# Kernel optimization log

Measured on AMD Instinct MI355X. Metric: run time of the kernel, lower is better.

Reference implementation:

```python
import jax, jax.numpy as jnp
import numpy as np

H = 512      # hidden_size
NH = 8       # head_size (num heads)
DH = H // NH # att_size per head
FFN = 2048
B, S = 8, 1024
NEG = -1e9
EPS = 1e-5


def _layernorm(x, g, b):
    mu = jnp.mean(x, axis=-1, keepdims=True)
    var = jnp.var(x, axis=-1, keepdims=True)
    return (x - mu) * jax.lax.rsqrt(var + EPS) * g + b


def setup_inputs() -> dict:
    key = jax.random.key(0)
    ks = jax.random.split(key, 16)
    s = 0.02
    return {
        "x": jax.random.normal(ks[0], (B, S, H), jnp.float32),
        "attn_bias": jax.random.normal(ks[1], (B, S, S), jnp.float32),
        "graph_mask": jax.random.randint(ks[2], (B, S, S), 0, 2, jnp.int32),
        "ln1_g": jnp.ones((H,), jnp.float32),
        "ln1_b": jnp.zeros((H,), jnp.float32),
        "Wq": jax.random.normal(ks[3], (H, H), jnp.float32) * s,
        "bq": jnp.zeros((H,), jnp.float32),
        "Wk": jax.random.normal(ks[4], (H, H), jnp.float32) * s,
        "bk": jnp.zeros((H,), jnp.float32),
        "Wv": jax.random.normal(ks[5], (H, H), jnp.float32) * s,
        "bv": jnp.zeros((H,), jnp.float32),
        "Wo": jax.random.normal(ks[6], (H, H), jnp.float32) * s,
        "bo": jnp.zeros((H,), jnp.float32),
        "ln2_g": jnp.ones((H,), jnp.float32),
        "ln2_b": jnp.zeros((H,), jnp.float32),
        "W1": jax.random.normal(ks[7], (H, FFN), jnp.float32) * s,
        "b1": jnp.zeros((FFN,), jnp.float32),
        "W2": jax.random.normal(ks[8], (FFN, H), jnp.float32) * s,
        "b2": jnp.zeros((H,), jnp.float32),
    }


def reference(x, attn_bias, graph_mask, ln1_g, ln1_b, Wq, bq, Wk, bk, Wv, bv,
              Wo, bo, ln2_g, ln2_b, W1, b1, W2, b2):
    b, s, h = x.shape
    # --- self-attention block (eval mode: dropouts are identity) ---
    y = _layernorm(x, ln1_g, ln1_b)
    q = (y @ Wq + bq).reshape(b, s, NH, DH).transpose(0, 2, 1, 3)  # [B,h,S,d]
    k = (y @ Wk + bk).reshape(b, s, NH, DH).transpose(0, 2, 1, 3)
    v = (y @ Wv + bv).reshape(b, s, NH, DH).transpose(0, 2, 1, 3)
    scale = DH ** -0.5
    scores = jnp.einsum('bhqd,bhkd->bhqk', q * scale, k)  # [B,h,S,S]
    mask = (graph_mask == 0)[:, None, :, :]               # [B,1,S,S] broadcast over heads
    bias = jnp.where(mask, NEG, attn_bias[:, None, :, :])
    scores = scores + bias
    scores = jnp.where(mask, NEG, scores)
    p = jax.nn.softmax(scores, axis=-1)
    o = jnp.einsum('bhqk,bhkd->bhqd', p, v)
    o = o.transpose(0, 2, 1, 3).reshape(b, s, h) @ Wo + bo
    x = x + o
    # --- FFN block ---
    y = _layernorm(x, ln2_g, ln2_b)
    y = jax.nn.gelu(y @ W1 + b1, approximate=False) @ W2 + b2
    return x + y
```

## Files before the change

kernel.cpp:

```cpp
#include <hip/hip_runtime.h>
#include <hip/hip_bf16.h>
#include <type_traits>

static constexpr int kS   = 1024;
static constexpr int kH   = 512;
static constexpr int kFFN = 2048;

using bf16 = __hip_bfloat16;
using short8  = __attribute__((ext_vector_type(8))) short;
using float4v = __attribute__((ext_vector_type(4))) float;
#define MFMA16 __builtin_amdgcn_mfma_f32_16x16x32_bf16

__device__ __forceinline__ unsigned short f2bfu(float f){
  unsigned int u = __float_as_uint(f);
  return (unsigned short)((u + 0x7fffu + ((u >> 16) & 1u)) >> 16);
}
__device__ __forceinline__ float bfu2f(unsigned short u){
  return __uint_as_float(((unsigned int)u) << 16);
}
__device__ __forceinline__ unsigned int pack2(float a, float b){
  return (unsigned int)f2bfu(a) | ((unsigned int)f2bfu(b) << 16);
}
__device__ __forceinline__ void async16(const void* g, void* l){
  __builtin_amdgcn_global_load_lds(
    (const __attribute__((address_space(1))) unsigned int*)g,
    (__attribute__((address_space(3))) unsigned int*)l, 16, 0, 0);
}
__device__ __forceinline__ int swz(int col, int row){
  return (col & ~63) | (((((col>>3)&7) ^ (row&7)))<<3) | (col&7);
}

__global__ __launch_bounds__(256) void ln_kernel(const float* __restrict__ x,
    const float* __restrict__ g, const float* __restrict__ bb, bf16* __restrict__ y){
  int wave = threadIdx.x >> 6, lane = threadIdx.x & 63;
  long row = (long)blockIdx.x * 4 + wave;
  const float* xr = x + row * kH + lane*8;
  float4 a = *(const float4*)xr, c = *(const float4*)(xr+4);
  float v[8] = {a.x,a.y,a.z,a.w,c.x,c.y,c.z,c.w};
  float s=0.f, s2=0.f;
#pragma unroll
  for(int i=0;i<8;i++){ s += v[i]; s2 += v[i]*v[i]; }
#pragma unroll
  for(int o=32; o>=1; o>>=1){ s += __shfl_xor(s,o,64); s2 += __shfl_xor(s2,o,64); }
  float mu  = s * (1.f/kH);
  float rs  = rsqrtf(s2*(1.f/kH) - mu*mu + 1e-5f);
  float gv[8], bv[8];
  {
    float4 t0=*(const float4*)(g+lane*8),  t1=*(const float4*)(g+lane*8+4);
    float4 t2=*(const float4*)(bb+lane*8), t3=*(const float4*)(bb+lane*8+4);
    gv[0]=t0.x;gv[1]=t0.y;gv[2]=t0.z;gv[3]=t0.w;gv[4]=t1.x;gv[5]=t1.y;gv[6]=t1.z;gv[7]=t1.w;
    bv[0]=t2.x;bv[1]=t2.y;bv[2]=t2.z;bv[3]=t2.w;bv[4]=t3.x;bv[5]=t3.y;bv[6]=t3.z;bv[7]=t3.w;
  }
  unsigned int ow[4];
#pragma unroll
  for(int i=0;i<4;i++){
    float a0 = (v[2*i]  -mu)*rs*gv[2*i]   + bv[2*i];
    float a1 = (v[2*i+1]-mu)*rs*gv[2*i+1] + bv[2*i+1];
    ow[i] = pack2(a0, a1);
  }
  *reinterpret_cast<uint4*>(y + row*kH + swz(lane*8, (int)row)) = make_uint4(ow[0],ow[1],ow[2],ow[3]);
}

__global__ __launch_bounds__(256) void prep_wt(const float* __restrict__ W,
    bf16* __restrict__ WT, int K, int N){
  __shared__ unsigned short Ts[64*68];
  int tid=threadIdx.x;
  int kb=blockIdx.y*64, nb=blockIdx.x*64;
  {
    int k=tid>>2, nc=(tid&3)*16;
    const float* p = W + (size_t)(kb+k)*N + nb+nc;
#pragma unroll
    for(int i=0;i<16;i+=4){
      float4 f = *(const float4*)(p+i);
      Ts[k*68+nc+i  ]=f2bfu(f.x); Ts[k*68+nc+i+1]=f2bfu(f.y);
      Ts[k*68+nc+i+2]=f2bfu(f.z); Ts[k*68+nc+i+3]=f2bfu(f.w);
    }
  }
  __syncthreads();
  {
    int n=tid>>2, kc=(tid&3)*16;
    unsigned short tmp[16];
#pragma unroll
    for(int i=0;i<16;i++) tmp[i] = Ts[(kc+i)*68 + n];
    int row = nb+n, kg0 = kc>>3;
    bf16* op = WT + (size_t)row*K + kb;
    *(uint4*)(op + (((kg0  ^(row&7)))<<3)) = *(uint4*)&tmp[0];
    *(uint4*)(op + ((((kg0+1)^(row&7)))<<3)) = *(uint4*)&tmp[8];
  }
}

__global__ __launch_bounds__(256) void concat3(const float* __restrict__ a,
    const float* __restrict__ b, const float* __restrict__ c, float* __restrict__ o){
  int i = blockIdx.x*256 + threadIdx.x;
  if(i < 1536) o[i] = i<512 ? a[i] : (i<1024 ? b[i-512] : c[i-1024]);
}

__global__ __launch_bounds__(256) void bias_eff_kernel(
    const int* __restrict__ mask, const float* __restrict__ bias, bf16* __restrict__ be){
  size_t i8 = ((size_t)blockIdx.x*256 + threadIdx.x)*8;
  int4   m0 = *(const int4*)(mask+i8),   m1 = *(const int4*)(mask+i8+4);
  float4 b0 = *(const float4*)(bias+i8), b1 = *(const float4*)(bias+i8+4);
  const unsigned short NEG = f2bfu(-1e9f);
  unsigned short o[8];
  o[0]=m0.x?f2bfu(b0.x):NEG; o[1]=m0.y?f2bfu(b0.y):NEG;
  o[2]=m0.z?f2bfu(b0.z):NEG; o[3]=m0.w?f2bfu(b0.w):NEG;
  o[4]=m1.x?f2bfu(b1.x):NEG; o[5]=m1.y?f2bfu(b1.y):NEG;
  o[6]=m1.z?f2bfu(b1.z):NEG; o[7]=m1.w?f2bfu(b1.w):NEG;
  *(uint4*)((unsigned short*)be + i8) = *(uint4*)o;
}

__global__ __launch_bounds__(256) void transpose_bf16(
    const bf16* __restrict__ v, bf16* __restrict__ vT, int R)
{
  __shared__ unsigned short Ts[64*72];
  int tid=threadIdx.x;
  int rb = blockIdx.y*64, cb = blockIdx.x*64;
  {
    int r=tid>>2, c=(tid&3)*16;
    const bf16* p = v + (size_t)(rb+r)*kH + cb + c;
    *(uint4*)(&Ts[r*72+c])   = *(const uint4*)p;
    *(uint4*)(&Ts[r*72+c+8]) = *(const uint4*)(p+8);
  }
  __syncthreads();
  {
    int c=tid>>2, kb=(tid&3)*16;
    unsigned short tmp[16];
#pragma unroll
    for(int i=0;i<16;i++) tmp[i] = Ts[(kb+i)*72 + c];
    bf16* op = vT + (size_t)(cb+c)*R + rb + kb;
    *(uint4*)(op)   = *(uint4*)(&tmp[0]);
    *(uint4*)(op+8) = *(uint4*)(&tmp[8]);
  }
}

template<int BM, int BN, typename OutT, bool SCALE, bool GELU, bool RES, bool CSW>
__global__ __launch_bounds__((BM/64)*(BN/64)*64, 3) void mfma_gemm(
    const bf16* __restrict__ A, const bf16* __restrict__ BT,
    const float* __restrict__ bias, const float* __restrict__ res,
    OutT* __restrict__ C, int M, int N, int K)
{
  constexpr int W  = (BM/64)*(BN/64);
  constexpr int NW = BN/64;
  constexpr int AC = (BM/8)/W, BC = (BN/8)/W;
  __shared__ __align__(16) unsigned short As[BM*64];
  __shared__ __align__(16) unsigned short Bs[BN*64];
  int tid=threadIdx.x, lane=tid&63, quad=lane>>4, l16=lane&15;
  int w=__builtin_amdgcn_readfirstlane(tid>>6);
  int wr = w / NW, wc = w % NW;
  int m0=blockIdx.y*BM, n0=blockIdx.x*BN;
  int lr=lane>>3, lc=lane&7;
  float4v acc[4][4] = {};
  for(int k0=0;k0<K;k0+=64){
    __syncthreads();
#pragma unroll
    for(int i=0;i<AC;i++){
      int r = (w*AC+i)*8;
      async16(A + (size_t)(m0+r+lr)*K + k0 + lc*8, &As[r*64]);
    }
#pragma unroll
    for(int i=0;i<BC;i++){
      int r = (w*BC+i)*8;
      async16(BT + (size_t)(n0+r+lr)*K + k0 + lc*8, &Bs[r*64]);
    }
    __syncthreads();
#pragma unroll
    for(int hf=0;hf<2;hf++){
      short8 af[4], bfv[4];
#pragma unroll
      for(int mi=0;mi<4;mi++){
        int row=wr*64+mi*16+l16;
        af[mi]=*(const short8*)&As[row*64 + (((hf*4+quad)^(row&7))<<3)];
      }
#pragma unroll
      for(int ni=0;ni<4;ni++){
        int n=wc*64+ni*16+l16;
        bfv[ni]=*(const short8*)&Bs[n*64 + (((hf*4+quad)^(n&7))<<3)];
      }
#pragma unroll
      for(int ni=0;ni<4;ni++)
#pragma unroll
        for(int mi=0;mi<4;mi++)
          acc[mi][ni]=MFMA16(af[mi],bfv[ni],acc[mi][ni],0,0,0);
    }
  }
#pragma unroll
  for(int ni=0;ni<4;ni++){
    int col=n0+wc*64+ni*16+l16;
    float bc=bias[col];
#pragma unroll
    for(int mi=0;mi<4;mi++){
#pragma unroll
      for(int r=0;r<4;r++){
        int row=m0+wr*64+mi*16+quad*4+r;
        float v=acc[mi][ni][r]+bc;
        if constexpr(SCALE) v*=0.125f;
        if constexpr(GELU)  v=0.5f*v*(1.f+erff(v*0.70710678118f));
        size_t idx=(size_t)row*N+col;
        if constexpr(RES) v+=res[idx];
        if constexpr(std::is_same<OutT,float>::value) C[idx]=v;
        else {
          size_t ix = CSW ? ((size_t)row*N + swz(col,row)) : idx;
          reinterpret_cast<unsigned short*>(C)[ix]=f2bfu(v);
        }
      }
    }
  }
}

__global__ __launch_bounds__(256, 3) void mfma_gemm_qkv(
    const bf16* __restrict__ A, const bf16* __restrict__ BT,
    const float* __restrict__ bias, bf16* __restrict__ qo,
    bf16* __restrict__ ko, bf16* __restrict__ vo, int M, int N, int K)
{
  __shared__ __align__(16) unsigned short As[128*64];
  __shared__ __align__(16) unsigned short Bs[128*64];
  int tid=threadIdx.x, lane=tid&63, quad=lane>>4, l16=lane&15;
  int w=__builtin_amdgcn_readfirstlane(tid>>6);
  int wr = w >> 1, wc = w & 1;
  int m0=blockIdx.y*128, n0=blockIdx.x*128;
  int lr=lane>>3, lc=lane&7;
  float4v acc[4][4] = {};
  for(int k0=0;k0<K;k0+=64){
    __syncthreads();
#pragma unroll
    for(int i=0;i<4;i++){
      int r = (w*4+i)*8;
      async16(A + (size_t)(m0+r+lr)*K + k0 + lc*8, &As[r*64]);
    }
#pragma unroll
    for(int i=0;i<4;i++){
      int r = (w*4+i)*8;
      async16(BT + (size_t)(n0+r+lr)*K + k0 + lc*8, &Bs[r*64]);
    }
    __syncthreads();
#pragma unroll
    for(int hf=0;hf<2;hf++){
      short8 af[4], bfv[4];
#pragma unroll
      for(int mi=0;mi<4;mi++){
        int row=wr*64+mi*16+l16;
        af[mi]=*(const short8*)&As[row*64 + (((hf*4+quad)^(row&7))<<3)];
      }
#pragma unroll
      for(int ni=0;ni<4;ni++){
        int n=wc*64+ni*16+l16;
        bfv[ni]=*(const short8*)&Bs[n*64 + (((hf*4+quad)^(n&7))<<3)];
      }
#pragma unroll
      for(int ni=0;ni<4;ni++)
#pragma unroll
        for(int mi=0;mi<4;mi++)
          acc[mi][ni]=MFMA16(af[mi],bfv[ni],acc[mi][ni],0,0,0);
    }
  }
  int sec = __builtin_amdgcn_readfirstlane(n0 >> 9);
  unsigned short* dst = (unsigned short*)(sec==0 ? qo : (sec==1 ? ko : vo));
  float scl = (sec==0) ? 0.125f : 1.0f;
#pragma unroll
  for(int ni=0;ni<4;ni++){
    int col=n0+wc*64+ni*16+l16;
    float bc=bias[col];
    int cl=col&511;
#pragma unroll
    for(int mi=0;mi<4;mi++){
#pragma unroll
      for(int r=0;r<4;r++){
        int row=m0+wr*64+mi*16+quad*4+r;
        dst[(size_t)row*512+cl]=f2bfu((acc[mi][ni][r]+bc)*scl);
      }
    }
  }
}

__global__ __launch_bounds__(256,2) void attn_mfma(
    const bf16* __restrict__ q, const bf16* __restrict__ k,
    const bf16* __restrict__ vT, const bf16* __restrict__ be,
    bf16* __restrict__ o)
{
  __shared__ __align__(16) unsigned short Ks[64*64];
  __shared__ __align__(16) unsigned short Vt[64*64];
  __shared__ __align__(16) unsigned short Bt[64*64];
  __shared__ __align__(16) unsigned short Ps[4*16*72];
  int tid=threadIdx.x, lane=tid&63, quad=lane>>4, l16=lane&15;
  int w=__builtin_amdgcn_readfirstlane(tid>>6);
  int q0=blockIdx.x*64, b=blockIdx.y>>3, h=blockIdx.y&7;
  int lr=lane>>3, lc=lane&7;
  const bf16* qp = q + (size_t)(b*kS + q0 + w*16 + l16)*kH + h*64;
  short8 aq0 = *(const short8*)(qp + quad*8);
  short8 aq1 = *(const short8*)(qp + 32 + quad*8);
  float lpart[4]={0.f,0.f,0.f,0.f};
  float4v oacc[4]={};
  int pb = w*16*72;
  int rql = w*16 + quad*4;
  for(int kt=0;kt<16;kt++){
    int kb=kt*64;
    __syncthreads();
#pragma unroll
    for(int i=0;i<2;i++){
      int rr = w*16 + i*8;
      async16(k  + (size_t)(b*kS+kb+rr+lr)*kH + h*64 + ((lc^lr)<<3), &Ks[rr*64]);
      async16(vT + (size_t)(h*64+rr+lr)*8192 + b*kS + kb + ((lc^lr)<<3), &Vt[rr*64]);
      async16(be + (size_t)(b*kS+q0+rr+lr)*kS + kb + ((lc^lr)<<3), &Bt[rr*64]);
    }
    __syncthreads();
    float4v sa[4];
#pragma unroll
    for(int t=0;t<4;t++){
      int krow=t*16+l16, kx=krow&7;
      short8 b0 = *(const short8*)&Ks[krow*64 + ((quad^kx)<<3)];
      short8 b1 = *(const short8*)&Ks[krow*64 + (((4+quad)^kx)<<3)];
      float4v ci;
#pragma unroll
      for(int r=0;r<4;r++){
        int row = rql + r;
        ci[r] = bfu2f(Bt[row*64 + (((t*2+(l16>>3)) ^ (row&7))<<3) + (l16&7)]);
      }
      ci = MFMA16(aq0,b0,ci,0,0,0);
      sa[t]=MFMA16(aq1,b1,ci,0,0,0);
    }
#pragma unroll
    for(int t=0;t<4;t++){
      int kg = t*2 + (l16>>3), j = l16&7;
#pragma unroll
      for(int r=0;r<4;r++){
        float p = __expf(sa[t][r] - 24.f);
        lpart[r] += p;
        int row = quad*4+r;
        Ps[pb + row*72 + ((kg^(row&7))<<3) + j] = f2bfu(p);
      }
    }
    short8 ap0 = *(const short8*)&Ps[pb + l16*72 + ((quad^(l16&7))<<3)];
    short8 ap1 = *(const short8*)&Ps[pb + l16*72 + (((4+quad)^(l16&7))<<3)];
#pragma unroll
    for(int dt=0;dt<4;dt++){
      int vrow=dt*16+l16, vx=vrow&7;
      short8 bv0=*(const short8*)&Vt[vrow*64+((quad^vx)<<3)];
      short8 bv1=*(const short8*)&Vt[vrow*64+(((4+quad)^vx)<<3)];
      oacc[dt]=MFMA16(ap0,bv0,oacc[dt],0,0,0);
      oacc[dt]=MFMA16(ap1,bv1,oacc[dt],0,0,0);
    }
  }
  float inv[4];
#pragma unroll
  for(int r=0;r<4;r++){
    float l = lpart[r];
    l += __shfl_xor(l,1,64); l += __shfl_xor(l,2,64);
    l += __shfl_xor(l,4,64); l += __shfl_xor(l,8,64);
    inv[r] = 1.f/l;
  }
#pragma unroll
  for(int dt=0;dt<4;dt++)
#pragma unroll
    for(int r=0;r<4;r++){
      int row = b*kS + q0 + rql + r;
      int col = h*64 + dt*16 + l16;
      reinterpret_cast<unsigned short*>(o)[(size_t)row*kH + swz(col,row)] =
        f2bfu(oacc[dt][r]*inv[r]);
    }
}

extern "C" void kernel_launch(void* const* d_in, const int* in_sizes, int n_in,
                              void* d_out, int out_size, void* d_ws, size_t ws_size,
                              hipStream_t stream){
  (void)in_sizes; (void)n_in; (void)out_size; (void)ws_size;
  const float* x         = (const float*)d_in[0];
  const float* attn_bias = (const float*)d_in[1];
  const int*   graph_mask= (const int*)  d_in[2];
  const float* ln1_g = (const float*)d_in[3];
  const float* ln1_b = (const float*)d_in[4];
  const float* Wq = (const float*)d_in[5];
  const float* bq = (const float*)d_in[6];
  const float* Wk = (const float*)d_in[7];
  const float* bk = (const float*)d_in[8];
  const float* Wv = (const float*)d_in[9];
  const float* bv = (const float*)d_in[10];
  const float* Wo = (const float*)d_in[11];
  const float* bo = (const float*)d_in[12];
  const float* ln2_g = (const float*)d_in[13];
  const float* ln2_b = (const float*)d_in[14];
  const float* W1 = (const float*)d_in[15];
  const float* b1 = (const float*)d_in[16];
  const float* W2 = (const float*)d_in[17];
  const float* b2 = (const float*)d_in[18];

  char* wsb = (char*)d_ws;
  const size_t SZ = (size_t)8192 * kH * sizeof(bf16);
  bf16* s0 = (bf16*)(wsb);
  bf16* s1 = (bf16*)(wsb + SZ);
  bf16* s2 = (bf16*)(wsb + 2*SZ);
  bf16* s3 = (bf16*)(wsb + 3*SZ);
  float* outf = (float*)d_out;
  bf16*  WqkvT = (bf16*)d_out;
  float* bqkv  = (float*)((char*)d_out + (2u<<20));
  bf16*  vraw  = (bf16*)((char*)d_out + (8u<<20));
  bf16*  beP   = (bf16*)d_out;
  bf16* WoT = s3;
  bf16* W1T = s3 + 262144;
  bf16* W2T = s3 + 262144 + 1048576;

  dim3 blk(256);
  prep_wt<<<dim3(8,8),  blk, 0, stream>>>(Wq, WqkvT,          kH, kH);
  prep_wt<<<dim3(8,8),  blk, 0, stream>>>(Wk, WqkvT + 262144, kH, kH);
  prep_wt<<<dim3(8,8),  blk, 0, stream>>>(Wv, WqkvT + 524288, kH, kH);
  concat3<<<dim3(6), blk, 0, stream>>>(bq, bk, bv, bqkv);
  ln_kernel<<<dim3(2048), blk, 0, stream>>>(x, ln1_g, ln1_b, s0);
  mfma_gemm_qkv<<<dim3(12,64), blk, 0, stream>>>(s0, WqkvT, bqkv, s1, s2, vraw, 8192, 3*kH, kH);
  transpose_bf16<<<dim3(8,128), blk, 0, stream>>>(vraw, s3, 8192);
  bias_eff_kernel<<<dim3(4096), blk, 0, stream>>>(graph_mask, attn_bias, beP);
  attn_mfma<<<dim3(16,64), blk, 0, stream>>>(s1, s2, s3, beP, s0);
  prep_wt<<<dim3(8,8), blk, 0, stream>>>(Wo, WoT, kH, kH);
  mfma_gemm<128,128,float,false,false,true,false><<<dim3(4,64), blk, 0, stream>>>(s0, WoT, bo, x, outf, 8192, kH, kH);
  ln_kernel<<<dim3(2048), blk, 0, stream>>>(outf, ln2_g, ln2_b, s0);
  prep_wt<<<dim3(32,8), blk, 0, stream>>>(W1, W1T, kH, kFFN);
  prep_wt<<<dim3(8,32), blk, 0, stream>>>(W2, W2T, kFFN, kH);
  for(int c=0;c<2;c++){
    size_t ro = (size_t)c * 4096 * kH;
    mfma_gemm<128,128,bf16,false,true ,false,true ><<<dim3(16,32), blk, 0, stream>>>(s0 + ro, W1T, b1, nullptr, s1, 4096, kFFN, kH);
    mfma_gemm<64,64,  float,false,false,true ,false><<<dim3(8,64),  dim3(64), 0, stream>>>(s1, W2T, b2, outf + ro, outf + ro, 4096, kH, kFFN);
  }
}
```

Measured before the change: 376.7 us.

## Fuse prep launches, write V transposed from QKV GEMM, retile Wo GEMM

Measured after the change: 349.1 us. -7.3%, faster.

```diff
diff --git a/kernel.cpp b/kernel.cpp
--- a/kernel.cpp
+++ b/kernel.cpp
@@ -30,10 +30,9 @@
   return (col & ~63) | (((((col>>3)&7) ^ (row&7)))<<3) | (col&7);
 }
 
-__global__ __launch_bounds__(256) void ln_kernel(const float* __restrict__ x,
-    const float* __restrict__ g, const float* __restrict__ bb, bf16* __restrict__ y){
-  int wave = threadIdx.x >> 6, lane = threadIdx.x & 63;
-  long row = (long)blockIdx.x * 4 + wave;
+__device__ __forceinline__ void ln_row(const float* __restrict__ x,
+    const float* __restrict__ g, const float* __restrict__ bb,
+    bf16* __restrict__ y, long row, int lane){
   const float* xr = x + row * kH + lane*8;
   float4 a = *(const float4*)xr, c = *(const float4*)(xr+4);
   float v[8] = {a.x,a.y,a.z,a.w,c.x,c.y,c.z,c.w};
@@ -61,11 +60,15 @@
   *reinterpret_cast<uint4*>(y + row*kH + swz(lane*8, (int)row)) = make_uint4(ow[0],ow[1],ow[2],ow[3]);
 }
 
-__global__ __launch_bounds__(256) void prep_wt(const float* __restrict__ W,
-    bf16* __restrict__ WT, int K, int N){
+__global__ __launch_bounds__(256) void ln_kernel(const float* __restrict__ x,
+    const float* __restrict__ g, const float* __restrict__ bb, bf16* __restrict__ y){
+  ln_row(x, g, bb, y, (long)blockIdx.x*4 + (threadIdx.x>>6), threadIdx.x&63);
+}
+
+__device__ __forceinline__ void prep_tile(const float* __restrict__ W,
+    bf16* __restrict__ WT, int K, int N, int kb, int nb){
   __shared__ unsigned short Ts[64*68];
   int tid=threadIdx.x;
-  int kb=blockIdx.y*64, nb=blockIdx.x*64;
   {
     int k=tid>>2, nc=(tid&3)*16;
     const float* p = W + (size_t)(kb+k)*N + nb+nc;
@@ -89,10 +92,29 @@
   }
 }
 
-__global__ __launch_bounds__(256) void concat3(const float* __restrict__ a,
-    const float* __restrict__ b, const float* __restrict__ c, float* __restrict__ o){
-  int i = blockIdx.x*256 + threadIdx.x;
-  if(i < 1536) o[i] = i<512 ? a[i] : (i<1024 ? b[i-512] : c[i-1024]);
+__global__ __launch_bounds__(256) void ln1_prep_qkv(
+    const float* __restrict__ x, const float* __restrict__ g, const float* __restrict__ bb,
+    bf16* __restrict__ y, const float* __restrict__ Wq, const float* __restrict__ Wk,
+    const float* __restrict__ Wv, bf16* __restrict__ WT){
+  int id = blockIdx.x;
+  if(id < 2048){
+    ln_row(x, g, bb, y, (long)id*4 + (threadIdx.x>>6), threadIdx.x&63);
+  } else {
+    int pid = id - 2048, sel = pid>>6, lid = pid&63;
+    const float* W = sel==0 ? Wq : (sel==1 ? Wk : Wv);
+    prep_tile(W, WT + (size_t)sel*262144, kH, kH, (lid>>3)*64, (lid&7)*64);
+  }
+}
+
+__global__ __launch_bounds__(256) void prep_rest(
+    const float* __restrict__ Wo, const float* __restrict__ W1, const float* __restrict__ W2,
+    bf16* __restrict__ WoT, bf16* __restrict__ W1T, bf16* __restrict__ W2T){
+  int id = blockIdx.x;
+  const float* W; bf16* WT; int K, N, kb, nb;
+  if(id < 64)       { W=Wo; WT=WoT; K=kH;   N=kH;   kb=(id>>3)*64;        nb=(id&7)*64; }
+  else if(id < 320) { int l=id-64;  W=W1; WT=W1T; K=kH;   N=kFFN; kb=(l>>5)*64; nb=(l&31)*64; }
+  else              { int l=id-320; W=W2; WT=W2T; K=kFFN; N=kH;   kb=(l>>3)*64; nb=(l&7)*64; }
+  prep_tile(W, WT, K, N, kb, nb);
 }
 
 __global__ __launch_bounds__(256) void bias_eff_kernel(
@@ -107,30 +129,6 @@
   o[4]=m1.x?f2bfu(b1.x):NEG; o[5]=m1.y?f2bfu(b1.y):NEG;
   o[6]=m1.z?f2bfu(b1.z):NEG; o[7]=m1.w?f2bfu(b1.w):NEG;
   *(uint4*)((unsigned short*)be + i8) = *(uint4*)o;
-}
-
-__global__ __launch_bounds__(256) void transpose_bf16(
-    const bf16* __restrict__ v, bf16* __restrict__ vT, int R)
-{
-  __shared__ unsigned short Ts[64*72];
-  int tid=threadIdx.x;
-  int rb = blockIdx.y*64, cb = blockIdx.x*64;
-  {
-    int r=tid>>2, c=(tid&3)*16;
-    const bf16* p = v + (size_t)(rb+r)*kH + cb + c;
-    *(uint4*)(&Ts[r*72+c])   = *(const uint4*)p;
-    *(uint4*)(&Ts[r*72+c+8]) = *(const uint4*)(p+8);
-  }
-  __syncthreads();
-  {
-    int c=tid>>2, kb=(tid&3)*16;
-    unsigned short tmp[16];
-#pragma unroll
-    for(int i=0;i<16;i++) tmp[i] = Ts[(kb+i)*72 + c];
-    bf16* op = vT + (size_t)(cb+c)*R + rb + kb;
-    *(uint4*)(op)   = *(uint4*)(&tmp[0]);
-    *(uint4*)(op+8) = *(uint4*)(&tmp[8]);
-  }
 }
 
 template<int BM, int BN, typename OutT, bool SCALE, bool GELU, bool RES, bool CSW>
@@ -209,8 +207,8 @@
 
 __global__ __launch_bounds__(256, 3) void mfma_gemm_qkv(
     const bf16* __restrict__ A, const bf16* __restrict__ BT,
-    const float* __restrict__ bias, bf16* __restrict__ qo,
-    bf16* __restrict__ ko, bf16* __restrict__ vo, int M, int N, int K)
+    const float* __restrict__ bq, const float* __restrict__ bk, const float* __restrict__ bv,
+    bf16* __restrict__ qo, bf16* __restrict__ ko, bf16* __restrict__ vT, int M, int N, int K)
 {
   __shared__ __align__(16) unsigned short As[128*64];
   __shared__ __align__(16) unsigned short Bs[128*64];
@@ -254,19 +252,35 @@
     }
   }
   int sec = __builtin_amdgcn_readfirstlane(n0 >> 9);
-  unsigned short* dst = (unsigned short*)(sec==0 ? qo : (sec==1 ? ko : vo));
-  float scl = (sec==0) ? 0.125f : 1.0f;
-#pragma unroll
-  for(int ni=0;ni<4;ni++){
-    int col=n0+wc*64+ni*16+l16;
-    float bc=bias[col];
-    int cl=col&511;
-#pragma unroll
-    for(int mi=0;mi<4;mi++){
-#pragma unroll
-      for(int r=0;r<4;r++){
-        int row=m0+wr*64+mi*16+quad*4+r;
-        dst[(size_t)row*512+cl]=f2bfu((acc[mi][ni][r]+bc)*scl);
+  const float* bp = sec==0 ? bq : (sec==1 ? bk : bv);
+  if(sec == 2){
+#pragma unroll
+    for(int ni=0;ni<4;ni++){
+      int cl=(n0+wc*64+ni*16+l16)&511;
+      float bc=bp[cl];
+#pragma unroll
+      for(int mi=0;mi<4;mi++){
+        int row0=m0+wr*64+mi*16+quad*4;
+        unsigned int p0=pack2(acc[mi][ni][0]+bc, acc[mi][ni][1]+bc);
+        unsigned int p1=pack2(acc[mi][ni][2]+bc, acc[mi][ni][3]+bc);
+        *reinterpret_cast<uint2*>(reinterpret_cast<unsigned short*>(vT)
+            + (size_t)cl*8192 + row0) = make_uint2(p0,p1);
+      }
+    }
+  } else {
+    unsigned short* dst = (unsigned short*)(sec==0 ? qo : ko);
+    float scl = (sec==0) ? 0.125f : 1.0f;
+#pragma unroll
+    for(int ni=0;ni<4;ni++){
+      int col=n0+wc*64+ni*16+l16, cl=col&511;
+      float bc=bp[cl];
+#pragma unroll
+      for(int mi=0;mi<4;mi++){
+#pragma unroll
+        for(int r=0;r<4;r++){
+          int row=m0+wr*64+mi*16+quad*4+r;
+          dst[(size_t)row*512+cl]=f2bfu((acc[mi][ni][r]+bc)*scl);
+        }
       }
     }
   }
@@ -391,28 +405,19 @@
   bf16* s3 = (bf16*)(wsb + 3*SZ);
   float* outf = (float*)d_out;
   bf16*  WqkvT = (bf16*)d_out;
-  float* bqkv  = (float*)((char*)d_out + (2u<<20));
-  bf16*  vraw  = (bf16*)((char*)d_out + (8u<<20));
   bf16*  beP   = (bf16*)d_out;
   bf16* WoT = s3;
   bf16* W1T = s3 + 262144;
   bf16* W2T = s3 + 262144 + 1048576;
 
   dim3 blk(256);
-  prep_wt<<<dim3(8,8),  blk, 0, stream>>>(Wq, WqkvT,          kH, kH);
-  prep_wt<<<dim3(8,8),  blk, 0, stream>>>(Wk, WqkvT + 262144, kH, kH);
-  prep_wt<<<dim3(8,8),  blk, 0, stream>>>(Wv, WqkvT + 524288, kH, kH);
-  concat3<<<dim3(6), blk, 0, stream>>>(bq, bk, bv, bqkv);
-  ln_kernel<<<dim3(2048), blk, 0, stream>>>(x, ln1_g, ln1_b, s0);
-  mfma_gemm_qkv<<<dim3(12,64), blk, 0, stream>>>(s0, WqkvT, bqkv, s1, s2, vraw, 8192, 3*kH, kH);
-  transpose_bf16<<<dim3(8,128), blk, 0, stream>>>(vraw, s3, 8192);
+  ln1_prep_qkv<<<dim3(2240), blk, 0, stream>>>(x, ln1_g, ln1_b, s0, Wq, Wk, Wv, WqkvT);
+  mfma_gemm_qkv<<<dim3(12,64), blk, 0, stream>>>(s0, WqkvT, bq, bk, bv, s1, s2, s3, 8192, 3*kH, kH);
   bias_eff_kernel<<<dim3(4096), blk, 0, stream>>>(graph_mask, attn_bias, beP);
   attn_mfma<<<dim3(16,64), blk, 0, stream>>>(s1, s2, s3, beP, s0);
-  prep_wt<<<dim3(8,8), blk, 0, stream>>>(Wo, WoT, kH, kH);
-  mfma_gemm<128,128,float,false,false,true,false><<<dim3(4,64), blk, 0, stream>>>(s0, WoT, bo, x, outf, 8192, kH, kH);
+  prep_rest<<<dim3(576), blk, 0, stream>>>(Wo, W1, W2, WoT, W1T, W2T);
+  mfma_gemm<128,64,float,false,false,true,false><<<dim3(8,64), dim3(128), 0, stream>>>(s0, WoT, bo, x, outf, 8192, kH, kH);
   ln_kernel<<<dim3(2048), blk, 0, stream>>>(outf, ln2_g, ln2_b, s0);
-  prep_wt<<<dim3(32,8), blk, 0, stream>>>(W1, W1T, kH, kFFN);
-  prep_wt<<<dim3(8,32), blk, 0, stream>>>(W2, W2T, kFFN, kH);
   for(int c=0;c<2;c++){
     size_t ro = (size_t)c * 4096 * kH;
     mfma_gemm<128,128,bf16,false,true ,false,true ><<<dim3(16,32), blk, 0, stream>>>(s0 + ro, W1T, b1, nullptr, s1, 4096, kFFN, kH);
```
